# Kernel tuning notes

Hardware: AMD Instinct MI355X
Metric: run time of the kernel (lower is better)

Reference implementation:

```python
import jax, jax.numpy as jnp
import numpy as np

B, T, C, H = 4, 2048, 1024, 16
D = C // H  # head dim = 64


def setup_inputs() -> dict:
    key = jax.random.key(0)
    k1, k2, k3 = jax.random.split(key, 3)
    scale = 0.02
    x = jax.random.normal(k1, (B, T, C), dtype=jnp.float32)
    Wqkv = jax.random.normal(k2, (C, 3 * C), dtype=jnp.float32) * scale
    bqkv = jnp.zeros((3 * C,), dtype=jnp.float32)
    Wproj = jax.random.normal(k3, (C, C), dtype=jnp.float32) * scale
    bproj = jnp.zeros((C,), dtype=jnp.float32)
    return {"x": x, "Wqkv": Wqkv, "bqkv": bqkv, "Wproj": Wproj, "bproj": bproj}


def reference(x, Wqkv, bqkv, Wproj, bproj):
    Bx, Tx, Cx = x.shape
    qkv = x @ Wqkv + bqkv  # [B,T,3C]
    q, k, v = jnp.split(qkv, 3, axis=2)
    # [B,T,C] -> [B,H,T,D]
    q = q.reshape(Bx, Tx, H, D).transpose(0, 2, 1, 3)
    k = k.reshape(Bx, Tx, H, D).transpose(0, 2, 1, 3)
    v = v.reshape(Bx, Tx, H, D).transpose(0, 2, 1, 3)
    scores = jnp.einsum('bhqd,bhkd->bhqk', q, k) * (D ** -0.5)
    causal = jnp.tril(jnp.ones((Tx, Tx), dtype=bool))
    scores = jnp.where(causal[None, None], scores, -jnp.inf)
    attn = jax.nn.softmax(scores, axis=-1)
    out = jnp.einsum('bhqk,bhkd->bhqd', attn, v)  # [B,H,T,D]
    out = out.transpose(0, 2, 1, 3).reshape(Bx, Tx, Cx)
    return out @ Wproj + bproj
```

## Files before the change

### kernel.cpp

```cpp
#include <hip/hip_runtime.h>
#include <stdint.h>

typedef __bf16 bf16x8 __attribute__((ext_vector_type(8)));
typedef float  f32x4  __attribute__((ext_vector_type(4)));
typedef short  s16x8  __attribute__((ext_vector_type(8)));

__device__ __forceinline__ unsigned short f2bf(float f) {
  unsigned u = __builtin_bit_cast(unsigned, f);
  u += 0x7fffu + ((u >> 16) & 1u);
  return (unsigned short)(u >> 16);
}

__device__ __forceinline__ bf16x8 ld8(const unsigned short* p) {
  return __builtin_bit_cast(bf16x8, *reinterpret_cast<const s16x8*>(p));
}

#define MFMA16(a,b,c) __builtin_amdgcn_mfma_f32_16x16x32_bf16((a),(b),(c),0,0,0)
#define EXP2(x) __builtin_amdgcn_exp2f(x)

#define BB 4
#define TT 2048
#define CC 1024
#define HH 16
#define DD 64
#define MM (BB*TT)

__global__ __launch_bounds__(256) void cvt_f32_bf16(const float* __restrict__ in,
                                                    unsigned short* __restrict__ out, int n) {
  int idx = blockIdx.x * blockDim.x + threadIdx.x;
  int stride = gridDim.x * blockDim.x;
  for (int i = idx * 4; i < n; i += stride * 4) {
    float4 v = *reinterpret_cast<const float4*>(in + i);
    ushort4 o;
    o.x = f2bf(v.x); o.y = f2bf(v.y); o.z = f2bf(v.z); o.w = f2bf(v.w);
    *reinterpret_cast<ushort4*>(out + i) = o;
  }
}

__global__ __launch_bounds__(256) void transpose_cvt(const float* __restrict__ in,
                                                     unsigned short* __restrict__ out,
                                                     int K, int N) {
  __shared__ float tile[32][33];
  int kb = blockIdx.y * 32, nb = blockIdx.x * 32;
  int tx = threadIdx.x, ty = threadIdx.y;
  for (int i = 0; i < 4; i++)
    tile[ty + i*8][tx] = in[(size_t)(kb + ty + i*8) * N + nb + tx];
  __syncthreads();
  for (int i = 0; i < 4; i++)
    out[(size_t)(nb + ty + i*8) * K + kb + tx] = f2bf(tile[tx][ty + i*8]);
}

template<int EPI>
__global__ __launch_bounds__(256)
void gemm_glds(const unsigned short* __restrict__ A, const unsigned short* __restrict__ Bt,
               const float* __restrict__ bias, int K,
               unsigned short* __restrict__ qbuf, unsigned short* __restrict__ kbuf,
               unsigned short* __restrict__ vtbuf, float* __restrict__ outf)
{
  __shared__ __attribute__((aligned(16))) unsigned short As[2][128 * 32];
  __shared__ __attribute__((aligned(16))) unsigned short Bs[2][128 * 32];
  const int tid  = threadIdx.x;
  const int lane = tid & 63;
  const int w    = tid >> 6;
  const int wr   = w >> 1, wc = w & 1;
  const int lo   = lane & 15, hi = lane >> 4;
  const int row0 = blockIdx.x * 128, col0 = blockIdx.y * 128;

  f32x4 acc[4][4];
  #pragma unroll
  for (int m = 0; m < 4; m++)
    for (int n = 0; n < 4; n++)
      for (int j = 0; j < 4; j++) acc[m][n][j] = 0.f;

  const int srow = lane >> 2;
  const int scol = (lane & 3) * 8;
  const unsigned short* Ab = A  + (size_t)(row0 + w*16 + srow) * K + scol;
  const unsigned short* Bb = Bt + (size_t)(col0 + w*16 + srow) * K + scol;

  const int NT = K >> 5;
  auto STAGE = [&](int buf, int k0) {
    #pragma unroll
    for (int i = 0; i < 2; i++) {
      __builtin_amdgcn_global_load_lds(
        (const __attribute__((address_space(1))) unsigned int*)(Ab + (size_t)(i*64) * K + k0),
        (__attribute__((address_space(3))) unsigned int*)(&As[buf][(i*64 + w*16) * 32]), 16, 0, 0);
      __builtin_amdgcn_global_load_lds(
        (const __attribute__((address_space(1))) unsigned int*)(Bb + (size_t)(i*64) * K + k0),
        (__attribute__((address_space(3))) unsigned int*)(&Bs[buf][(i*64 + w*16) * 32]), 16, 0, 0);
    }
  };

  STAGE(0, 0);
  int cur = 0;
  for (int t = 0; t < NT; t++) {
    __syncthreads();
    if (t + 1 < NT) STAGE(cur ^ 1, (t + 1) * 32);

    bf16x8 af[4], bfr[4];
    #pragma unroll
    for (int m = 0; m < 4; m++)
      af[m] = ld8(&As[cur][(wr*64 + m*16 + lo) * 32 + hi*8]);
    #pragma unroll
    for (int n = 0; n < 4; n++)
      bfr[n] = ld8(&Bs[cur][(wc*64 + n*16 + lo) * 32 + hi*8]);
    #pragma unroll
    for (int m = 0; m < 4; m++)
      #pragma unroll
      for (int n = 0; n < 4; n++)
        acc[m][n] = MFMA16(af[m], bfr[n], acc[m][n]);
    cur ^= 1;
  }

  if (EPI == 0) {
    const int sec = col0 >> 10;
    #pragma unroll
    for (int m = 0; m < 4; m++) {
      int rbase = row0 + wr*64 + m*16 + hi*4;
      #pragma unroll
      for (int n = 0; n < 4; n++) {
        int c  = col0 + wc*64 + n*16 + lo;
        int cc = c & 1023;
        int h  = cc >> 6, d = cc & 63;
        float bv = bias[c];
        #pragma unroll
        for (int i = 0; i < 4; i++) {
          int r = rbase + i;
          int b = r >> 11, t = r & 2047;
          int bh = b * HH + h;
          unsigned short val = f2bf(acc[m][n][i] + bv);
          if (sec == 0)      qbuf [((size_t)bh * TT + t) * DD + d] = val;
          else if (sec == 1) kbuf [((size_t)bh * TT + t) * DD + d] = val;
          else               vtbuf[((size_t)bh * DD + d) * TT + t] = val;
        }
      }
    }
  } else {
    #pragma unroll
    for (int m = 0; m < 4; m++) {
      int rbase = row0 + wr*64 + m*16 + hi*4;
      #pragma unroll
      for (int n = 0; n < 4; n++) {
        int c = col0 + wc*64 + n*16 + lo;
        float bv = bias[c];
        #pragma unroll
        for (int i = 0; i < 4; i++)
          outf[(size_t)(rbase + i) * CC + c] = acc[m][n][i] + bv;
      }
    }
  }
}

#define PLD 88

__global__ __launch_bounds__(256)
void attn_kernel(const unsigned short* __restrict__ qbuf,
                 const unsigned short* __restrict__ kbuf,
                 const unsigned short* __restrict__ vtbuf,
                 unsigned short* __restrict__ obuf)
{
  __shared__ unsigned short P[4][32 * PLD];
  const int tid  = threadIdx.x;
  const int lane = tid & 63;
  const int w    = tid >> 6;
  const int lo   = lane & 15, hi = lane >> 4;
  const int bh   = blockIdx.x;
  const int qblk = gridDim.y - 1 - blockIdx.y;
  const int qbase = qblk * 128 + w * 32;
  const float SCL = 0.125f * 1.44269504088896f;

  const unsigned short* Kb = kbuf  + (size_t)bh * TT * DD;
  const unsigned short* Vb = vtbuf + (size_t)bh * DD * TT;

  bf16x8 aq[2][2];
  #pragma unroll
  for (int st = 0; st < 2; st++) {
    const unsigned short* qp = qbuf + ((size_t)bh * TT + qbase + st*16 + lo) * DD + hi * 8;
    bf16x8 q0 = ld8(qp), q1 = ld8(qp + 32);
    #pragma unroll
    for (int jj = 0; jj < 8; jj++) {
      q0[jj] = (__bf16)((float)q0[jj] * SCL);
      q1[jj] = (__bf16)((float)q1[jj] * SCL);
    }
    aq[st][0] = q0; aq[st][1] = q1;
  }

  float lrow[2][4];
  f32x4 acc_o[2][4];
  #pragma unroll
  for (int st = 0; st < 2; st++)
    for (int i = 0; i < 4; i++) {
      lrow[st][i] = 0.f;
      for (int f = 0; f < 4; f++) acc_o[st][f][i] = 0.f;
    }

  __bf16* Pw = (__bf16*)&P[w][0];
  const unsigned short* Pwu = &P[w][0];
  const int nfull = qbase >> 6;

  auto QK = [&](int kb2, f32x4 (&so)[2][4]) {
    #pragma unroll
    for (int st = 0; st < 2; st++)
      for (int f = 0; f < 4; f++)
        for (int i = 0; i < 4; i++) so[st][f][i] = 0.f;
    __builtin_amdgcn_s_setprio(1);
    #pragma unroll
    for (int f = 0; f < 4; f++) {
      const unsigned short* kp = Kb + (size_t)(kb2 + f*16 + lo) * DD + hi * 8;
      bf16x8 b0 = ld8(kp);
      bf16x8 b1 = ld8(kp + 32);
      so[0][f] = MFMA16(aq[0][0], b0, so[0][f]);
      so[0][f] = MFMA16(aq[0][1], b1, so[0][f]);
      so[1][f] = MFMA16(aq[1][0], b0, so[1][f]);
      so[1][f] = MFMA16(aq[1][1], b1, so[1][f]);
    }
    __builtin_amdgcn_s_setprio(0);
  };

  auto PV = [&](int kbase) {
    bf16x8 pa[2][2];
    #pragma unroll
    for (int st = 0; st < 2; st++) {
      pa[st][0] = ld8(Pwu + (st*16 + lo) * PLD + hi * 8);
      pa[st][1] = ld8(Pwu + (st*16 + lo) * PLD + 32 + hi * 8);
    }
    __builtin_amdgcn_s_setprio(1);
    #pragma unroll
    for (int f = 0; f < 4; f++) {
      const unsigned short* vp = Vb + (size_t)(f*16 + lo) * TT + kbase + hi * 8;
      bf16x8 v0 = ld8(vp);
      bf16x8 v1 = ld8(vp + 32);
      acc_o[0][f] = MFMA16(pa[0][0], v0, acc_o[0][f]);
      acc_o[0][f] = MFMA16(pa[0][1], v1, acc_o[0][f]);
      acc_o[1][f] = MFMA16(pa[1][0], v0, acc_o[1][f]);
      acc_o[1][f] = MFMA16(pa[1][1], v1, acc_o[1][f]);
    }
    __builtin_amdgcn_s_setprio(0);
  };

  f32x4 s[2][4];

  for (int kt = 0; kt < nfull; ++kt) {
    QK(kt*64, s);
    #pragma unroll
    for (int st = 0; st < 2; st++)
      #pragma unroll
      for (int f = 0; f < 4; f++)
        #pragma unroll
        for (int i = 0; i < 4; i++) {
          float p = EXP2(s[st][f][i]);
          lrow[st][i] += p;
          Pw[(st*16 + hi*4 + i) * PLD + f*16 + lo] = (__bf16)p;
        }
    PV(kt*64);
  }

  {
    const int kbase = nfull * 64;
    QK(kbase, s);
    #pragma unroll
    for (int st = 0; st < 2; st++) {
      const int rowoff = qbase + st*16 + hi*4;
      #pragma unroll
      for (int f = 0; f < 4; f++)
        #pragma unroll
        for (int i = 0; i < 4; i++) {
          bool mk = (kbase + f*16 + lo > rowoff + i);
          float p = mk ? 0.f : EXP2(s[st][f][i]);
          lrow[st][i] += p;
          Pw[(st*16 + hi*4 + i) * PLD + f*16 + lo] = (__bf16)p;
        }
    }
    PV(kbase);
  }

  #pragma unroll
  for (int xm = 1; xm < 16; xm <<= 1)
    #pragma unroll
    for (int st = 0; st < 2; st++)
      for (int i = 0; i < 4; i++)
        lrow[st][i] += __shfl_xor(lrow[st][i], xm);

  const int b = bh >> 4, h = bh & 15;
  __bf16* ob = (__bf16*)obuf;
  #pragma unroll
  for (int st = 0; st < 2; st++)
    for (int f = 0; f < 4; f++)
      for (int i = 0; i < 4; i++) {
        int r = qbase + st*16 + hi*4 + i;
        float v = acc_o[st][f][i] / lrow[st][i];
        ob[((size_t)(b * TT + r)) * CC + h*64 + f*16 + lo] = (__bf16)v;
      }
}

extern "C" void kernel_launch(void* const* d_in, const int* in_sizes, int n_in,
                              void* d_out, int out_size, void* d_ws, size_t ws_size,
                              hipStream_t stream) {
  const float* x     = (const float*)d_in[0];
  const float* Wqkv  = (const float*)d_in[1];
  const float* bqkv  = (const float*)d_in[2];
  const float* Wproj = (const float*)d_in[3];
  const float* bproj = (const float*)d_in[4];
  float* out = (float*)d_out;

  unsigned short* ws  = (unsigned short*)d_ws;
  unsigned short* xb  = ws;
  unsigned short* w1t = xb  + (size_t)MM * CC;
  unsigned short* w2t = w1t + (size_t)3 * CC * CC;
  unsigned short* qbf = w2t + (size_t)CC * CC;
  unsigned short* kbf = qbf + (size_t)BB * HH * TT * DD;
  unsigned short* vtb = kbf + (size_t)BB * HH * TT * DD;
  unsigned short* obf = xb;

  cvt_f32_bf16<<<2048, 256, 0, stream>>>(x, xb, MM * CC);
  transpose_cvt<<<dim3(3*CC/32, CC/32), dim3(32, 8), 0, stream>>>(Wqkv, w1t, CC, 3*CC);
  transpose_cvt<<<dim3(CC/32,  CC/32), dim3(32, 8), 0, stream>>>(Wproj, w2t, CC, CC);

  gemm_glds<0><<<dim3(MM/128, 3*CC/128), 256, 0, stream>>>(xb, w1t, bqkv, CC,
                                                           qbf, kbf, vtb, nullptr);
  attn_kernel<<<dim3(BB*HH, TT/128), 256, 0, stream>>>(qbf, kbf, vtb, obf);
  gemm_glds<1><<<dim3(MM/128, CC/128), 256, 0, stream>>>(obf, w2t, bproj, CC,
                                                         nullptr, nullptr, nullptr, out);
}
```

Measured before the change: 337.4 us.

## Stage K/V tiles in double-buffered shared memory shared across attention waves

```diff
diff --git a/kernel.cpp b/kernel.cpp
--- a/kernel.cpp
+++ b/kernel.cpp
@@ -150,26 +150,35 @@
   }
 }
 
-#define PLD 88
-
-__global__ __launch_bounds__(256)
+#define KLD 68
+#define PLD 72
+
+__global__ __launch_bounds__(256, 4)
 void attn_kernel(const unsigned short* __restrict__ qbuf,
                  const unsigned short* __restrict__ kbuf,
                  const unsigned short* __restrict__ vtbuf,
                  unsigned short* __restrict__ obuf)
 {
-  __shared__ unsigned short P[4][32 * PLD];
+  __shared__ __attribute__((aligned(16))) unsigned short Ks[2][64 * KLD];
+  __shared__ __attribute__((aligned(16))) unsigned short Vs[2][64 * KLD];
+  __shared__ __attribute__((aligned(16))) unsigned short Ps[4][32 * PLD];
   const int tid  = threadIdx.x;
   const int lane = tid & 63;
   const int w    = tid >> 6;
   const int lo   = lane & 15, hi = lane >> 4;
   const int bh   = blockIdx.x;
   const int qblk = gridDim.y - 1 - blockIdx.y;
-  const int qbase = qblk * 128 + w * 32;
+  const int qb_blk = qblk * 128;
+  const int qbase  = qb_blk + w * 32;
+  const int myDiag = qbase >> 6;
+  const int nlast  = (qb_blk + 127) >> 6;
   const float SCL = 0.125f * 1.44269504088896f;
 
   const unsigned short* Kb = kbuf  + (size_t)bh * TT * DD;
   const unsigned short* Vb = vtbuf + (size_t)bh * DD * TT;
+
+  const int r_l = lane >> 3;
+  const int c_l = (lane & 7) * 8;
 
   bf16x8 aq[2][2];
   #pragma unroll
@@ -193,84 +202,110 @@
       for (int f = 0; f < 4; f++) acc_o[st][f][i] = 0.f;
     }
 
-  __bf16* Pw = (__bf16*)&P[w][0];
-  const unsigned short* Pwu = &P[w][0];
-  const int nfull = qbase >> 6;
-
-  auto QK = [&](int kb2, f32x4 (&so)[2][4]) {
-    #pragma unroll
-    for (int st = 0; st < 2; st++)
-      for (int f = 0; f < 4; f++)
-        for (int i = 0; i < 4; i++) so[st][f][i] = 0.f;
-    __builtin_amdgcn_s_setprio(1);
-    #pragma unroll
-    for (int f = 0; f < 4; f++) {
-      const unsigned short* kp = Kb + (size_t)(kb2 + f*16 + lo) * DD + hi * 8;
-      bf16x8 b0 = ld8(kp);
-      bf16x8 b1 = ld8(kp + 32);
-      so[0][f] = MFMA16(aq[0][0], b0, so[0][f]);
-      so[0][f] = MFMA16(aq[0][1], b1, so[0][f]);
-      so[1][f] = MFMA16(aq[1][0], b0, so[1][f]);
-      so[1][f] = MFMA16(aq[1][1], b1, so[1][f]);
-    }
-    __builtin_amdgcn_s_setprio(0);
-  };
-
-  auto PV = [&](int kbase) {
-    bf16x8 pa[2][2];
-    #pragma unroll
-    for (int st = 0; st < 2; st++) {
-      pa[st][0] = ld8(Pwu + (st*16 + lo) * PLD + hi * 8);
-      pa[st][1] = ld8(Pwu + (st*16 + lo) * PLD + 32 + hi * 8);
-    }
-    __builtin_amdgcn_s_setprio(1);
-    #pragma unroll
-    for (int f = 0; f < 4; f++) {
-      const unsigned short* vp = Vb + (size_t)(f*16 + lo) * TT + kbase + hi * 8;
-      bf16x8 v0 = ld8(vp);
-      bf16x8 v1 = ld8(vp + 32);
-      acc_o[0][f] = MFMA16(pa[0][0], v0, acc_o[0][f]);
-      acc_o[0][f] = MFMA16(pa[0][1], v1, acc_o[0][f]);
-      acc_o[1][f] = MFMA16(pa[1][0], v0, acc_o[1][f]);
-      acc_o[1][f] = MFMA16(pa[1][1], v1, acc_o[1][f]);
-    }
-    __builtin_amdgcn_s_setprio(0);
-  };
-
-  f32x4 s[2][4];
-
-  for (int kt = 0; kt < nfull; ++kt) {
-    QK(kt*64, s);
-    #pragma unroll
-    for (int st = 0; st < 2; st++)
-      #pragma unroll
-      for (int f = 0; f < 4; f++)
+  __bf16* Pw = (__bf16*)&Ps[w][0];
+  const unsigned short* Pwu = &Ps[w][0];
+
+  {
+    s16x8 k0 = *reinterpret_cast<const s16x8*>(Kb + (size_t)(w*16 + r_l)     * DD + c_l);
+    s16x8 k1 = *reinterpret_cast<const s16x8*>(Kb + (size_t)(w*16 + 8 + r_l) * DD + c_l);
+    s16x8 v0 = *reinterpret_cast<const s16x8*>(Vb + (size_t)(w*16 + r_l)     * TT + c_l);
+    s16x8 v1 = *reinterpret_cast<const s16x8*>(Vb + (size_t)(w*16 + 8 + r_l) * TT + c_l);
+    *reinterpret_cast<s16x8*>(&Ks[0][(w*16 + r_l)     * KLD + c_l]) = k0;
+    *reinterpret_cast<s16x8*>(&Ks[0][(w*16 + 8 + r_l) * KLD + c_l]) = k1;
+    *reinterpret_cast<s16x8*>(&Vs[0][(w*16 + r_l)     * KLD + c_l]) = v0;
+    *reinterpret_cast<s16x8*>(&Vs[0][(w*16 + 8 + r_l) * KLD + c_l]) = v1;
+  }
+  __syncthreads();
+
+  int cur = 0;
+  for (int kt = 0; kt <= nlast; ++kt) {
+    const int kbase = kt * 64;
+    const bool havenext = (kt < nlast);
+    const bool act = (kt <= myDiag);
+
+    s16x8 kr0, kr1, vr0, vr1;
+    if (havenext) {
+      const int kb2 = kbase + 64;
+      kr0 = *reinterpret_cast<const s16x8*>(Kb + (size_t)(kb2 + w*16 + r_l)     * DD + c_l);
+      kr1 = *reinterpret_cast<const s16x8*>(Kb + (size_t)(kb2 + w*16 + 8 + r_l) * DD + c_l);
+      vr0 = *reinterpret_cast<const s16x8*>(Vb + (size_t)(w*16 + r_l)     * TT + kb2 + c_l);
+      vr1 = *reinterpret_cast<const s16x8*>(Vb + (size_t)(w*16 + 8 + r_l) * TT + kb2 + c_l);
+    }
+
+    f32x4 s[2][4];
+    if (act) {
+      #pragma unroll
+      for (int st = 0; st < 2; st++)
+        for (int f = 0; f < 4; f++)
+          for (int i = 0; i < 4; i++) s[st][f][i] = 0.f;
+      __builtin_amdgcn_s_setprio(1);
+      #pragma unroll
+      for (int f = 0; f < 4; f++) {
+        bf16x8 b0 = ld8(&Ks[cur][(f*16 + lo) * KLD + hi*8]);
+        bf16x8 b1 = ld8(&Ks[cur][(f*16 + lo) * KLD + 32 + hi*8]);
+        s[0][f] = MFMA16(aq[0][0], b0, s[0][f]);
+        s[0][f] = MFMA16(aq[0][1], b1, s[0][f]);
+        s[1][f] = MFMA16(aq[1][0], b0, s[1][f]);
+        s[1][f] = MFMA16(aq[1][1], b1, s[1][f]);
+      }
+      __builtin_amdgcn_s_setprio(0);
+
+      if (kt == myDiag) {
         #pragma unroll
-        for (int i = 0; i < 4; i++) {
-          float p = EXP2(s[st][f][i]);
-          lrow[st][i] += p;
-          Pw[(st*16 + hi*4 + i) * PLD + f*16 + lo] = (__bf16)p;
+        for (int st = 0; st < 2; st++) {
+          const int rowoff = qbase + st*16 + hi*4;
+          #pragma unroll
+          for (int f = 0; f < 4; f++)
+            for (int i = 0; i < 4; i++) {
+              bool mk = (kbase + f*16 + lo > rowoff + i);
+              float p = mk ? 0.f : EXP2(s[st][f][i]);
+              lrow[st][i] += p;
+              Pw[(st*16 + hi*4 + i) * PLD + f*16 + lo] = (__bf16)p;
+            }
         }
-    PV(kt*64);
-  }
-
-  {
-    const int kbase = nfull * 64;
-    QK(kbase, s);
-    #pragma unroll
-    for (int st = 0; st < 2; st++) {
-      const int rowoff = qbase + st*16 + hi*4;
-      #pragma unroll
-      for (int f = 0; f < 4; f++)
+      } else {
         #pragma unroll
-        for (int i = 0; i < 4; i++) {
-          bool mk = (kbase + f*16 + lo > rowoff + i);
-          float p = mk ? 0.f : EXP2(s[st][f][i]);
-          lrow[st][i] += p;
-          Pw[(st*16 + hi*4 + i) * PLD + f*16 + lo] = (__bf16)p;
-        }
-    }
-    PV(kbase);
+        for (int st = 0; st < 2; st++)
+          #pragma unroll
+          for (int f = 0; f < 4; f++)
+            #pragma unroll
+            for (int i = 0; i < 4; i++) {
+              float p = EXP2(s[st][f][i]);
+              lrow[st][i] += p;
+              Pw[(st*16 + hi*4 + i) * PLD + f*16 + lo] = (__bf16)p;
+            }
+      }
+    }
+
+    if (havenext) {
+      *reinterpret_cast<s16x8*>(&Ks[cur^1][(w*16 + r_l)     * KLD + c_l]) = kr0;
+      *reinterpret_cast<s16x8*>(&Ks[cur^1][(w*16 + 8 + r_l) * KLD + c_l]) = kr1;
+      *reinterpret_cast<s16x8*>(&Vs[cur^1][(w*16 + r_l)     * KLD + c_l]) = vr0;
+      *reinterpret_cast<s16x8*>(&Vs[cur^1][(w*16 + 8 + r_l) * KLD + c_l]) = vr1;
+    }
+
+    if (act) {
+      bf16x8 pa[2][2];
+      #pragma unroll
+      for (int st = 0; st < 2; st++) {
+        pa[st][0] = ld8(Pwu + (st*16 + lo) * PLD + hi*8);
+        pa[st][1] = ld8(Pwu + (st*16 + lo) * PLD + 32 + hi*8);
+      }
+      __builtin_amdgcn_s_setprio(1);
+      #pragma unroll
+      for (int f = 0; f < 4; f++) {
+        bf16x8 v0 = ld8(&Vs[cur][(f*16 + lo) * KLD + hi*8]);
+        bf16x8 v1 = ld8(&Vs[cur][(f*16 + lo) * KLD + 32 + hi*8]);
+        acc_o[0][f] = MFMA16(pa[0][0], v0, acc_o[0][f]);
+        acc_o[0][f] = MFMA16(pa[0][1], v1, acc_o[0][f]);
+        acc_o[1][f] = MFMA16(pa[1][0], v0, acc_o[1][f]);
+        acc_o[1][f] = MFMA16(pa[1][1], v1, acc_o[1][f]);
+      }
+      __builtin_amdgcn_s_setprio(0);
+    }
+
+    __syncthreads();
+    cur ^= 1;
   }
 
   #pragma unroll
```

Measured after the change: 367.3 us. +8.9%, slower.
